# Kernel optimization log

Measured on AMD Instinct MI355X. Metric: run time of the kernel, lower is better.

The kernel has to match this reference:

```python
import jax, jax.numpy as jnp
import numpy as np

K = 10  # knn_graph default k
NEG_SLOPE = 0.2


def _knn_idx(x, k):
    # x: (B, N, C) -> idx (B, N, k) of nearest neighbors (excluding self)
    x2 = jnp.sum(x * x, axis=-1)                       # (B, N)
    d = x2[:, :, None] + x2[:, None, :] - 2.0 * jnp.einsum('bnc,bmc->bnm', x, x)
    _, idx = jax.lax.top_k(-d, k + 1)                  # smallest distances
    return idx[:, :, 1:]                               # drop self


def _edge_conv(x, W, s, t, k):
    # x: (B, N, C); W: (O, 2C); s,t: (O,) folded BN scale/bias
    idx = _knn_idx(x, k)                               # (B, N, k)
    neigh = jax.vmap(lambda xb, ib: xb[ib])(x, idx)    # (B, N, k, C)
    xi = jnp.broadcast_to(x[:, :, None, :], neigh.shape)
    edge = jnp.concatenate([neigh - xi, xi], axis=-1)  # (B, N, k, 2C)
    h = jnp.einsum('bnkc,oc->bnko', edge, W) * s + t
    h = jnp.where(h >= 0, h, NEG_SLOPE * h)            # LeakyReLU(0.2)
    return jnp.max(h, axis=2)                          # max over neighbors -> (B, N, O)


def setup_inputs() -> dict:
    key = jax.random.key(0)
    ks = jax.random.split(key, 32)
    B, N = 8, 2048
    NC = 3
    def w(k_, shape):
        fan_in = shape[-1]
        return jax.random.normal(k_, shape, jnp.float32) * (1.0 / np.sqrt(fan_in))
    def sb(k_, c):  # positive scale, small bias
        k1, k2 = jax.random.split(k_)
        return (jax.random.uniform(k1, (c,), jnp.float32, 0.5, 1.5),
                jax.random.normal(k2, (c,), jnp.float32) * 0.1)
    points = jax.random.normal(ks[0], (B, N, 3), jnp.float32)
    W1 = w(ks[1], (64, 6));    s1, t1 = sb(ks[2], 64)
    W2 = w(ks[3], (64, 128));  s2, t2 = sb(ks[4], 64)
    W3 = w(ks[5], (128, 128)); s3, t3 = sb(ks[6], 128)
    W4 = w(ks[7], (256, 256)); s4, t4 = sb(ks[8], 256)
    W5 = w(ks[9], (1024, 512)); s5, t5 = sb(ks[10], 1024)
    Wf1 = w(ks[11], (512, 1024)); sf1, tf1 = sb(ks[12], 512)
    Wf2 = w(ks[13], (256, 512)); bf2 = jax.random.normal(ks[14], (256,), jnp.float32) * 0.02
    sf2, tf2 = sb(ks[15], 256)
    Wf3 = w(ks[16], (NC, 256)); bf3 = jax.random.normal(ks[17], (NC,), jnp.float32) * 0.02
    return {
        'points': points,
        'W1': W1, 's1': s1, 't1': t1,
        'W2': W2, 's2': s2, 't2': t2,
        'W3': W3, 's3': s3, 't3': t3,
        'W4': W4, 's4': s4, 't4': t4,
        'W5': W5, 's5': s5, 't5': t5,
        'Wf1': Wf1, 'sf1': sf1, 'tf1': tf1,
        'Wf2': Wf2, 'bf2': bf2, 'sf2': sf2, 'tf2': tf2,
        'Wf3': Wf3, 'bf3': bf3,
    }


def reference(points, W1, s1, t1, W2, s2, t2, W3, s3, t3, W4, s4, t4,
              W5, s5, t5, Wf1, sf1, tf1, Wf2, bf2, sf2, tf2, Wf3, bf3):
    lrelu = lambda h: jnp.where(h >= 0, h, NEG_SLOPE * h)
    out1 = _edge_conv(points, W1, s1, t1, K)   # (B, N, 64)
    out2 = _edge_conv(out1, W2, s2, t2, K)     # (B, N, 64)
    out3 = _edge_conv(out2, W3, s3, t3, K)     # (B, N, 128)
    out4 = _edge_conv(out3, W4, s4, t4, K)     # (B, N, 256)
    x = jnp.concatenate([out1, out2, out3, out4], axis=-1)  # (B, N, 512)
    h = lrelu(jnp.einsum('bnc,oc->bno', x, W5) * s5 + t5)   # (B, N, 1024)
    h = jnp.max(h, axis=1)                                  # global max pool -> (B, 1024)
    h = lrelu((h @ Wf1.T) * sf1 + tf1)                      # (B, 512); dropout=identity (eval)
    h = lrelu((h @ Wf2.T + bf2) * sf2 + tf2)                # (B, 256)
    return h @ Wf3.T + bf3                                  # (B, num_classes)
```

## Files before the change

### kernel.cpp

```cpp
#include <hip/hip_runtime.h>
#include <hip/hip_bf16.h>


#define NEG 0.2f
#define FMAX 3.402823466e+38f
#define KINIT 0x7F7FFFFFFFFFFFFFull

typedef __hip_bfloat16 bf16;
typedef __attribute__((ext_vector_type(8))) short s8v;
typedef __attribute__((ext_vector_type(4))) float f32x4;
typedef unsigned long long u64;

#define BB 8
#define NN 2048
#define BNTOT (BB * NN)
#define NPART 4

#define OFF_NORMS ((size_t)0)
#define OFF_PART (OFF_NORMS + BNTOT)
#define OFF_POOLED (OFF_PART + 8 * 1024 * 32)
#define OFF_H1 (OFF_POOLED + 8 * 1024)
#define OFF_H2 (OFF_H1 + 8 * 512)
#define WSF_TOTAL (OFF_H2 + 8 * 256)

#define WB1 0
#define WB2 4096
#define WB3 12288
#define WB4 28672
#define WTOT 94208

__device__ float g_ws_f[WSF_TOTAL];
__device__ float g_G[(size_t)8 * BNTOT * 64];
__device__ u64 g_pk[(size_t)BNTOT * NPART * 10];
__device__ int g_flag;
__device__ unsigned short g_hi[(size_t)BNTOT * 512];
__device__ unsigned short g_lo[(size_t)BNTOT * 512];
__device__ unsigned short g_xhi5[(size_t)BNTOT * 512];
__device__ unsigned short g_xlo5[(size_t)BNTOT * 512];
__device__ unsigned short g_whi[1024 * 512];
__device__ unsigned short g_wlo[1024 * 512];
__device__ unsigned short g_wfh[WTOT];
__device__ unsigned short g_wfl[WTOT];

__device__ __forceinline__ float ldany(const void* p, size_t i, int isb) {
  if (isb) return __bfloat162float(((const bf16*)p)[i]);
  return ((const float*)p)[i];
}

__global__ void probe_kernel(const void* pts) {
  const unsigned* w = (const unsigned*)pts;
  int cnt = 0;
  for (int i = 0; i < 256; ++i) {
    unsigned e2 = (w[i] >> 7) & 0xFF;
    cnt += (e2 >= 110 && e2 <= 135);
  }
  g_flag = (cnt > 128) ? 1 : 0;
}

__global__ void norms_kernel(const void* xraw, int lda, int C, int BN) {
  const int isb = g_flag;
  float* norms = g_ws_f + OFF_NORMS;
  int row = blockIdx.x * (blockDim.x >> 6) + (threadIdx.x >> 6);
  int lane = threadIdx.x & 63;
  if (row >= BN) return;
  float s = 0.f;
  for (int c = lane; c < C; c += 64) {
    float v = ldany(xraw, (size_t)row * lda + c, isb);
    s += v * v;
  }
#pragma unroll
  for (int off = 32; off > 0; off >>= 1) s += __shfl_down(s, off, 64);
  if (lane == 0) norms[row] = s;
}

__global__ void zero_norms() {
  int i = blockIdx.x * blockDim.x + threadIdx.x;
  if (i < BNTOT) g_ws_f[OFF_NORMS + i] = 0.f;
}

__global__ void split_kernel(const void* xraw, int lda, int C,
                             int csh2, int dst, int total) {
  int i = blockIdx.x * blockDim.x + threadIdx.x;
  if (i >= total) return;
  const int isb = g_flag;
  int t = i >> 9, win = i & 511;
  int quad = win >> 7, l16 = (win >> 3) & 15, j = win & 7;
  int ktiles_m1 = (1 << csh2) - 1;
  int rg = t >> csh2, kt = t & ktiles_m1;
  int r = rg * 16 + l16;
  int c = kt * 32 + quad * 8 + j;
  float v = (c < C) ? ldany(xraw, (size_t)r * lda + c, isb) : 0.f;
  bf16 h = __float2bfloat16(v);
  float hf = __bfloat162float(h);
  bf16 l = __float2bfloat16(v - hf);
  unsigned short* H = dst ? g_whi : g_hi;
  unsigned short* L = dst ? g_wlo : g_lo;
  H[i] = *(unsigned short*)&h;
  L[i] = *(unsigned short*)&l;
}

__global__ void split_w(const void* W, int C, int ktsh, int wbase, int whalf,
                        int total) {
  int i = blockIdx.x * blockDim.x + threadIdx.x;
  if (i >= total) return;
  int z = blockIdx.y;
  const int isb = g_flag;
  int t = i >> 9, win = i & 511;
  int quad = win >> 7, l16 = (win >> 3) & 15, j = win & 7;
  int rg = t >> ktsh, kt = t & ((1 << ktsh) - 1);
  int orow = rg * 16 + l16;
  int c = kt * 32 + quad * 8 + j;
  float v = (c < C) ? ldany(W, (size_t)orow * (2 * C) + (size_t)z * C + c, isb) : 0.f;
  bf16 h = __float2bfloat16(v);
  float hf = __bfloat162float(h);
  bf16 l = __float2bfloat16(v - hf);
  g_wfh[wbase + z * whalf + i] = *(unsigned short*)&h;
  g_wfl[wbase + z * whalf + i] = *(unsigned short*)&l;
}

template <int CPAD>
__global__ __launch_bounds__(256) void knn_fused(int N) {
  constexpr int KT = CPAD >> 5;
  __shared__ __align__(16) float sdbuf[2][64 * 68];
  __shared__ float th_sh[4][64];
  const int tid = threadIdx.x;
  const int wave = tid >> 6, lane = tid & 63;
  const int quad = lane >> 4, l16 = lane & 15;
  const int b = blockIdx.y;
  const int q0 = blockIdx.x * 64;
  const int part = blockIdx.z;
  const int PN = N / NPART;
  const int rowb = b * N;
  const float* norms = g_ws_f + OFF_NORMS;

  const int arg = ((rowb + q0) >> 4) + wave;
  s8v ah[KT], al[KT];
#pragma unroll
  for (int kt = 0; kt < KT; ++kt) {
    const int abase = (arg * KT + kt) * 512 + lane * 8;
    ah[kt] = *(const s8v*)(g_hi + abase);
    al[kt] = *(const s8v*)(g_lo + abase);
  }

  const int selfn = q0 + lane;
  const float qn = norms[rowb + selfn];
  u64 K[10];
#pragma unroll
  for (int i = 0; i < 10; ++i) K[i] = KINIT;
  th_sh[wave][lane] = FMAX;

  int pb = 0;
  for (int m0 = part * PN; m0 < (part + 1) * PN; m0 += 64, pb ^= 1) {
    float nmv[4];
#pragma unroll
    for (int s = 0; s < 4; ++s) nmv[s] = norms[rowb + m0 + s * 16 + l16];
    f32x4 acc[4];
#pragma unroll
    for (int s = 0; s < 4; ++s) acc[s] = (f32x4){0.f, 0.f, 0.f, 0.f};
    const int brg0 = (rowb + m0) >> 4;
    const int btile = brg0 * (KT * 512) + lane * 8;
#pragma unroll
    for (int kt = 0; kt < KT; ++kt) {
#pragma unroll
      for (int s = 0; s < 4; ++s) {
        const int boff = btile + (s * KT + kt) * 512;
        s8v bh = *(const s8v*)(g_hi + boff);
        s8v bl = *(const s8v*)(g_lo + boff);
        acc[s] = __builtin_amdgcn_mfma_f32_16x16x32_bf16(ah[kt], bh, acc[s], 0, 0, 0);
        acc[s] = __builtin_amdgcn_mfma_f32_16x16x32_bf16(ah[kt], bl, acc[s], 0, 0, 0);
        acc[s] = __builtin_amdgcn_mfma_f32_16x16x32_bf16(al[kt], bh, acc[s], 0, 0, 0);
      }
    }
    float* sd = sdbuf[pb];
#pragma unroll
    for (int s = 0; s < 4; ++s) {
      int ml = s * 16 + l16;
#pragma unroll
      for (int r = 0; r < 4; ++r)
        sd[(wave * 16 + quad * 4 + r) * 68 + ml] = nmv[s] - 2.f * acc[s][r];
    }
    __syncthreads();
    float T = fminf(fminf(th_sh[0][lane], th_sh[1][lane]),
                    fminf(th_sh[2][lane], th_sh[3][lane]));
    T = fminf(T, __uint_as_float((unsigned)(K[9] >> 32)));
    const float Tq = T - qn;
    const int mbase = m0 + wave * 16;
    const float* srow = sd + lane * 68 + wave * 16;
    unsigned pass = 0;
#pragma unroll
    for (int jj = 0; jj < 16; jj += 4) {
      float4 d4 = *(const float4*)(srow + jj);
      pass |= (unsigned)(d4.x <= Tq) << jj;
      pass |= (unsigned)(d4.y <= Tq) << (jj + 1);
      pass |= (unsigned)(d4.z <= Tq) << (jj + 2);
      pass |= (unsigned)(d4.w <= Tq) << (jj + 3);
    }
    if ((unsigned)(selfn - mbase) < 16u) pass &= ~(1u << (selfn - mbase));
    while (pass) {
      int jj = __builtin_ctz(pass);
      pass &= pass - 1;
      int m = mbase + jj;
      float d = fmaxf(srow[jj] + qn, 0.f);
      u64 key = ((u64)__float_as_uint(d) << 32) | (unsigned)m;
      if (key < K[9]) {
        bool prev = true;
#pragma unroll
        for (int s2 = 9; s2 >= 1; --s2) {
          bool sh = key < K[s2 - 1];
          K[s2] = sh ? K[s2 - 1] : (prev ? key : K[s2]);
          prev = sh;
        }
        if (prev) K[0] = key;
      }
    }
    th_sh[wave][lane] = __uint_as_float((unsigned)(K[9] >> 32));
  }
  __syncthreads();
  u64* mlist = (u64*)sdbuf;
#pragma unroll
  for (int i = 0; i < 10; ++i) mlist[(lane * 4 + wave) * 10 + i] = K[i];
  __syncthreads();
  if (tid < 64) {
    int q = tid;
    int p0 = 0, p1 = 0, p2 = 0, p3 = 0;
    size_t ob = ((size_t)(rowb + q0 + q) * NPART + part) * 10;
    for (int cnt = 0; cnt < 10; ++cnt) {
      u64 k0 = mlist[(q * 4 + 0) * 10 + p0];
      u64 k1 = mlist[(q * 4 + 1) * 10 + p1];
      u64 k2 = mlist[(q * 4 + 2) * 10 + p2];
      u64 k3 = mlist[(q * 4 + 3) * 10 + p3];
      u64 bk = k0; int bp = 0;
      if (k1 < bk) { bk = k1; bp = 1; }
      if (k2 < bk) { bk = k2; bp = 2; }
      if (k3 < bk) { bk = k3; bp = 3; }
      if (bp == 0) ++p0; else if (bp == 1) ++p1; else if (bp == 2) ++p2; else ++p3;
      g_pk[ob + cnt] = bk;
    }
  }
}

template <int CPAD>
__global__ __launch_bounds__(256) void gmat_mfma(int wbase, int whalf, int BN) {
  constexpr int KT = CPAD >> 5;
  const int tid = threadIdx.x;
  const int wave = tid >> 6, lane = tid & 63;
  const int quad = lane >> 4, l16 = lane & 15;
  const int r0 = blockIdx.x * 64;
  const int chunk = blockIdx.y;
  const int z = blockIdx.z;
  const int wz = wbase + z * whalf;
  const int wrg0 = chunk * 4;
  f32x4 acc[4];
#pragma unroll
  for (int s = 0; s < 4; ++s) acc[s] = (f32x4){0.f, 0.f, 0.f, 0.f};
  const int arg = (r0 >> 4) + wave;
#pragma unroll
  for (int kt = 0; kt < KT; ++kt) {
    const int abase = (arg * KT + kt) * 512 + lane * 8;
    s8v ah = *(const s8v*)(g_hi + abase);
    s8v al = *(const s8v*)(g_lo + abase);
#pragma unroll
    for (int s = 0; s < 4; ++s) {
      const int woff = wz + ((wrg0 + s) * KT + kt) * 512 + lane * 8;
      s8v bh = *(const s8v*)(g_wfh + woff);
      s8v bl = *(const s8v*)(g_wfl + woff);
      acc[s] = __builtin_amdgcn_mfma_f32_16x16x32_bf16(ah, bh, acc[s], 0, 0, 0);
      acc[s] = __builtin_amdgcn_mfma_f32_16x16x32_bf16(ah, bl, acc[s], 0, 0, 0);
      acc[s] = __builtin_amdgcn_mfma_f32_16x16x32_bf16(al, bh, acc[s], 0, 0, 0);
    }
  }
  float* Gz = g_G + (size_t)(chunk * 2 + z) * BN * 64;
#pragma unroll
  for (int s = 0; s < 4; ++s)
#pragma unroll
    for (int r = 0; r < 4; ++r)
      Gz[(r0 + wave * 16 + quad * 4 + r) * 64 + s * 16 + l16] = acc[s][r];
}

__global__ void edge_epi64(const void* s, const void* t, int colbase,
                           int knn_csh2, int norms_mode, int BN, int N) {
  __shared__ u64 kbuf[4][40];
  __shared__ int oidx[4][10];
  const int isb = g_flag;
  int tid = threadIdx.x;
  int p = tid >> 6, o = tid & 63;
  int row = blockIdx.x * 4 + p;
  int chunk = blockIdx.y;
  const float* G1 = g_G + (size_t)(chunk * 2 + 0) * BN * 64;
  const float* G2 = g_G + (size_t)(chunk * 2 + 1) * BN * 64;
  int b = row / N;
  if (o < 40) kbuf[p][o] = g_pk[(size_t)row * 40 + o];
  if (o < 40) {
    u64 myk = kbuf[p][o];
    int rank = 0;
#pragma unroll 8
    for (int j = 0; j < 40; ++j) rank += (kbuf[p][j] < myk);
    if (rank < 10) oidx[p][rank] = (int)(myk & 0xFFFFFFFFu);
  }
  float g1n = G1[row * 64 + o];
  float base = G2[row * 64 + o] - g1n;
  int co = chunk * 64 + o;
  float sv = ldany(s, co, isb), tv = ldany(t, co, isb);
  float mx = -FMAX;
  const int bn64 = b * N * 64;
#pragma unroll
  for (int k = 0; k < 10; ++k) {
    int m = oidx[p][k];
    m = (m < 0) ? 0 : ((m >= N) ? N - 1 : m);
    float h = sv * (G1[bn64 + m * 64 + o] + base) + tv;
    h = (h >= 0.f) ? h : NEG * h;
    mx = fmaxf(mx, h);
  }
  bf16 h16 = __float2bfloat16(mx);
  float hf = __bfloat162float(h16);
  bf16 l16v = __float2bfloat16(mx - hf);
  unsigned short hu = *(unsigned short*)&h16;
  unsigned short lu = *(unsigned short*)&l16v;
  if (knn_csh2 >= 0) {
    int KTL = 1 << knn_csh2;
    int ki = ((row >> 4) * KTL + (co >> 5)) * 512 +
             ((co >> 3) & 3) * 128 + (row & 15) * 8 + (co & 7);
    g_hi[ki] = hu; g_lo[ki] = lu;
  }
  {
    int gc = colbase + co;
    int wi = ((row >> 4) * 16 + (gc >> 5)) * 512 +
             ((gc >> 3) & 3) * 128 + (row & 15) * 8 + (gc & 7);
    g_xhi5[wi] = hu; g_xlo5[wi] = lu;
  }
  if (norms_mode) {
    float ns = mx * mx;
#pragma unroll
    for (int off = 32; off > 0; off >>= 1) ns += __shfl_down(ns, off, 64);
    if (o == 0) {
      if (norms_mode == 1) g_ws_f[OFF_NORMS + row] = ns;
      else atomicAdd(&g_ws_f[OFF_NORMS + row], ns);
    }
  }
}

__global__ __launch_bounds__(256) void w5max_mfma(const void* s5, const void* t5, int N) {
  const int tid = threadIdx.x;
  const int wave = tid >> 6, lane = tid & 63;
  const int quad = lane >> 4, l16 = lane & 15;
  const int b = blockIdx.z;
  const int o0 = blockIdx.y * 64, n0 = blockIdx.x * 256;
  f32x4 acc[4][4];
#pragma unroll
  for (int a = 0; a < 4; ++a)
#pragma unroll
    for (int s = 0; s < 4; ++s) acc[a][s] = (f32x4){0.f, 0.f, 0.f, 0.f};

  const int arg0 = ((b * N + n0) >> 4) + wave * 4;
  const int wrg0 = o0 >> 4;
  for (int kt = 0; kt < 16; ++kt) {
    s8v ah[4], al[4];
#pragma unroll
    for (int a = 0; a < 4; ++a) {
      const int abase = ((arg0 + a) * 16 + kt) * 512 + lane * 8;
      ah[a] = *(const s8v*)(g_xhi5 + abase);
      al[a] = *(const s8v*)(g_xlo5 + abase);
    }
#pragma unroll
    for (int s = 0; s < 4; ++s) {
      const int bbase = ((wrg0 + s) * 16 + kt) * 512 + lane * 8;
      s8v bh = *(const s8v*)(g_whi + bbase);
      s8v bl = *(const s8v*)(g_wlo + bbase);
#pragma unroll
      for (int a = 0; a < 4; ++a) {
        acc[a][s] = __builtin_amdgcn_mfma_f32_16x16x32_bf16(ah[a], bh, acc[a][s], 0, 0, 0);
        acc[a][s] = __builtin_amdgcn_mfma_f32_16x16x32_bf16(ah[a], bl, acc[a][s], 0, 0, 0);
        acc[a][s] = __builtin_amdgcn_mfma_f32_16x16x32_bf16(al[a], bh, acc[a][s], 0, 0, 0);
      }
    }
  }
  __shared__ float red[4][64];
  const int isb = g_flag;
#pragma unroll
  for (int s = 0; s < 4; ++s) {
    float m4 = -FMAX;
#pragma unroll
    for (int a = 0; a < 4; ++a)
#pragma unroll
      for (int r = 0; r < 4; ++r) m4 = fmaxf(m4, acc[a][s][r]);
#pragma unroll
    for (int off = 16; off < 64; off <<= 1) m4 = fmaxf(m4, __shfl_down(m4, off, 64));
    if (quad == 0) red[wave][s * 16 + l16] = m4;
  }
  __syncthreads();
  if (tid < 64) {
    float m = fmaxf(fmaxf(red[0][tid], red[1][tid]), fmaxf(red[2][tid], red[3][tid]));
    int o = o0 + tid;
    float sv = ldany(s5, o, isb), tv = ldany(t5, o, isb);
    float h = sv * m + tv;
    h = (h >= 0.f) ? h : NEG * h;
    g_ws_f[OFF_PART + ((size_t)b * 1024 + o) * 8 + blockIdx.x] = h;
  }
}

__global__ void poolred_kernel() {
  const float* part = g_ws_f + OFF_PART;
  float* pooled = g_ws_f + OFF_POOLED;
  int i = blockIdx.x * blockDim.x + threadIdx.x;
  if (i >= 8 * 1024) return;
  const float* p = part + (size_t)i * 8;
  float m = -FMAX;
#pragma unroll
  for (int j = 0; j < 8; ++j) m = fmaxf(m, p[j]);
  pooled[i] = m;
}

__global__ void fc_kernel(size_t inoff, const void* W, const void* bias,
                          const void* s, const void* t, size_t outoff, int has_out,
                          void* OUTB, int Bb, int IC, int OC, int act) {
  const int isb = g_flag;
  const float* IN = g_ws_f + inoff;
  int gw = (blockIdx.x * blockDim.x + threadIdx.x) >> 6;
  int lane = threadIdx.x & 63;
  if (gw >= Bb * OC) return;
  int b = gw / OC, o = gw % OC;
  const float* in = IN + (size_t)b * IC;
  float acc = 0.f;
  for (int c = lane; c < IC; c += 64) acc += in[c] * ldany(W, (size_t)o * IC + c, isb);
#pragma unroll
  for (int off = 32; off > 0; off >>= 1) acc += __shfl_down(acc, off, 64);
  if (lane == 0) {
    float h = acc;
    if (bias) h += ldany(bias, o, isb);
    if (s) h = h * ldany(s, o, isb) + ldany(t, o, isb);
    if (act) h = (h >= 0.f) ? h : NEG * h;
    if (has_out) g_ws_f[outoff + (size_t)b * OC + o] = h;
    if (OUTB) {
      if (isb) ((bf16*)OUTB)[(size_t)b * OC + o] = __float2bfloat16(h);
      else ((float*)OUTB)[(size_t)b * OC + o] = h;
    }
  }
}

extern "C" void kernel_launch(void* const* d_in, const int* in_sizes, int n_in,
                              void* d_out, int out_size, void* d_ws, size_t ws_size,
                              hipStream_t stream) {
  const int B = 8, N = 2048, BN = B * N;
  const void* points = d_in[0];
  const void *W1 = d_in[1], *s1 = d_in[2], *t1 = d_in[3];
  const void *W2 = d_in[4], *s2 = d_in[5], *t2 = d_in[6];
  const void *W3 = d_in[7], *s3 = d_in[8], *t3 = d_in[9];
  const void *W4 = d_in[10], *s4 = d_in[11], *t4 = d_in[12];
  const void *W5 = d_in[13], *s5 = d_in[14], *t5 = d_in[15];
  const void *Wf1 = d_in[16], *sf1 = d_in[17], *tf1 = d_in[18];
  const void *Wf2 = d_in[19], *bf2 = d_in[20], *sf2 = d_in[21], *tf2 = d_in[22];
  const void *Wf3 = d_in[23], *bf3 = d_in[24];

  probe_kernel<<<1, 1, 0, stream>>>(points);
  split_kernel<<<(1024 * 512) / 256, 256, 0, stream>>>(W5, 512, 512, 4, 1, 1024 * 512);
  split_w<<<dim3(2048 / 256, 2), 256, 0, stream>>>(W1, 3, 0, WB1, 2048, 2048);
  split_w<<<dim3(4096 / 256, 2), 256, 0, stream>>>(W2, 64, 1, WB2, 4096, 4096);
  split_w<<<dim3(8192 / 256, 2), 256, 0, stream>>>(W3, 64, 1, WB3, 8192, 8192);
  split_w<<<dim3(32768 / 256, 2), 256, 0, stream>>>(W4, 128, 2, WB4, 32768, 32768);

  norms_kernel<<<BN / 4, 256, 0, stream>>>(points, 3, 3, BN);
  split_kernel<<<(BN * 32) / 256, 256, 0, stream>>>(points, 3, 3, 0, 0, BN * 32);
  knn_fused<32><<<dim3(N / 64, B, NPART), 256, 0, stream>>>(N);
  gmat_mfma<32><<<dim3(BN / 64, 1, 2), 256, 0, stream>>>(WB1, 2048, BN);
  edge_epi64<<<dim3(BN / 4, 1), 256, 0, stream>>>(s1, t1, 0, 1, 1, BN, N);
  knn_fused<64><<<dim3(N / 64, B, NPART), 256, 0, stream>>>(N);
  gmat_mfma<64><<<dim3(BN / 64, 1, 2), 256, 0, stream>>>(WB2, 4096, BN);
  edge_epi64<<<dim3(BN / 4, 1), 256, 0, stream>>>(s2, t2, 64, 1, 1, BN, N);
  knn_fused<64><<<dim3(N / 64, B, NPART), 256, 0, stream>>>(N);
  gmat_mfma<64><<<dim3(BN / 64, 2, 2), 256, 0, stream>>>(WB3, 8192, BN);
  zero_norms<<<BN / 256, 256, 0, stream>>>();
  edge_epi64<<<dim3(BN / 4, 2), 256, 0, stream>>>(s3, t3, 128, 2, 2, BN, N);
  knn_fused<128><<<dim3(N / 64, B, NPART), 256, 0, stream>>>(N);
  gmat_mfma<128><<<dim3(BN / 64, 4, 2), 256, 0, stream>>>(WB4, 32768, BN);
  edge_epi64<<<dim3(BN / 4, 4), 256, 0, stream>>>(s4, t4, 256, -1, 0, BN, N);
  w5max_mfma<<<dim3(8, 16, 8), 256, 0, stream>>>(s5, t5, N);
  poolred_kernel<<<32, 256, 0, stream>>>();
  fc_kernel<<<(8 * 512 * 64) / 256, 256, 0, stream>>>(OFF_POOLED, Wf1, nullptr, sf1, tf1, OFF_H1, 1, nullptr, 8, 1024, 512, 1);
  fc_kernel<<<(8 * 256 * 64) / 256, 256, 0, stream>>>(OFF_H1, Wf2, bf2, sf2, tf2, OFF_H2, 1, nullptr, 8, 512, 256, 1);
  fc_kernel<<<6, 256, 0, stream>>>(OFF_H2, Wf3, bf3, nullptr, nullptr, 0, 0, d_out, 8, 256, 3, 0);
}
```

Before: 559.4 us.

## Select kNN candidates directly from MFMA registers without shared-memory distance staging

The distance MFMA now swaps its operands so that each lane's accumulator holds distances for one query across several candidates. Each lane keeps a top-10 list per query and candidate-quad, filtered by a threshold shared through wave shuffles. This removes the shared-memory distance tile, the per-tile __syncthreads, and the cross-wave threshold array. In exchange it keeps four partial lists per query that must be merged at the end, and the filter branch may diverge more within a wave.

```diff
diff --git a/kernel.cpp b/kernel.cpp
--- a/kernel.cpp
+++ b/kernel.cpp
@@ -118,11 +118,24 @@
   g_wfl[wbase + z * whalf + i] = *(unsigned short*)&l;
 }
 
+__device__ __forceinline__ void insert10(u64* K, float d, int m) {
+  u64 key = ((u64)__float_as_uint(fmaxf(d, 0.f)) << 32) | (unsigned)m;
+  if (key < K[9]) {
+    bool prev = true;
+#pragma unroll
+    for (int s2 = 9; s2 >= 1; --s2) {
+      bool sh = key < K[s2 - 1];
+      K[s2] = sh ? K[s2 - 1] : (prev ? key : K[s2]);
+      prev = sh;
+    }
+    if (prev) K[0] = key;
+  }
+}
+
 template <int CPAD>
 __global__ __launch_bounds__(256) void knn_fused(int N) {
   constexpr int KT = CPAD >> 5;
-  __shared__ __align__(16) float sdbuf[2][64 * 68];
-  __shared__ float th_sh[4][64];
+  __shared__ __align__(16) u64 mbuf[4][16 * 4 * 10];
   const int tid = threadIdx.x;
   const int wave = tid >> 6, lane = tid & 63;
   const int quad = lane >> 4, l16 = lane & 15;
@@ -133,102 +146,75 @@
   const int rowb = b * N;
   const float* norms = g_ws_f + OFF_NORMS;
 
-  const int arg = ((rowb + q0) >> 4) + wave;
-  s8v ah[KT], al[KT];
+  const int qrg = ((rowb + q0) >> 4) + wave;
+  s8v qh[KT], ql[KT];
 #pragma unroll
   for (int kt = 0; kt < KT; ++kt) {
-    const int abase = (arg * KT + kt) * 512 + lane * 8;
-    ah[kt] = *(const s8v*)(g_hi + abase);
-    al[kt] = *(const s8v*)(g_lo + abase);
-  }
-
-  const int selfn = q0 + lane;
-  const float qn = norms[rowb + selfn];
+    const int qbase = (qrg * KT + kt) * 512 + lane * 8;
+    qh[kt] = *(const s8v*)(g_hi + qbase);
+    ql[kt] = *(const s8v*)(g_lo + qbase);
+  }
+
+  const int selfq = q0 + wave * 16 + l16;
+  const float qn = norms[rowb + selfq];
   u64 K[10];
 #pragma unroll
   for (int i = 0; i < 10; ++i) K[i] = KINIT;
-  th_sh[wave][lane] = FMAX;
-
-  int pb = 0;
-  for (int m0 = part * PN; m0 < (part + 1) * PN; m0 += 64, pb ^= 1) {
-    float nmv[4];
-#pragma unroll
-    for (int s = 0; s < 4; ++s) nmv[s] = norms[rowb + m0 + s * 16 + l16];
+
+  for (int m0 = part * PN; m0 < (part + 1) * PN; m0 += 64) {
+    f32x4 nmv[4];
+#pragma unroll
+    for (int s = 0; s < 4; ++s)
+      nmv[s] = *(const f32x4*)(norms + rowb + m0 + s * 16 + quad * 4);
     f32x4 acc[4];
 #pragma unroll
     for (int s = 0; s < 4; ++s) acc[s] = (f32x4){0.f, 0.f, 0.f, 0.f};
-    const int brg0 = (rowb + m0) >> 4;
-    const int btile = brg0 * (KT * 512) + lane * 8;
+    const int mrg0 = (rowb + m0) >> 4;
 #pragma unroll
     for (int kt = 0; kt < KT; ++kt) {
 #pragma unroll
       for (int s = 0; s < 4; ++s) {
-        const int boff = btile + (s * KT + kt) * 512;
-        s8v bh = *(const s8v*)(g_hi + boff);
-        s8v bl = *(const s8v*)(g_lo + boff);
-        acc[s] = __builtin_amdgcn_mfma_f32_16x16x32_bf16(ah[kt], bh, acc[s], 0, 0, 0);
-        acc[s] = __builtin_amdgcn_mfma_f32_16x16x32_bf16(ah[kt], bl, acc[s], 0, 0, 0);
-        acc[s] = __builtin_amdgcn_mfma_f32_16x16x32_bf16(al[kt], bh, acc[s], 0, 0, 0);
+        const int moff = ((mrg0 + s) * KT + kt) * 512 + lane * 8;
+        s8v mh = *(const s8v*)(g_hi + moff);
+        s8v ml = *(const s8v*)(g_lo + moff);
+        acc[s] = __builtin_amdgcn_mfma_f32_16x16x32_bf16(mh, qh[kt], acc[s], 0, 0, 0);
+        acc[s] = __builtin_amdgcn_mfma_f32_16x16x32_bf16(ml, qh[kt], acc[s], 0, 0, 0);
+        acc[s] = __builtin_amdgcn_mfma_f32_16x16x32_bf16(mh, ql[kt], acc[s], 0, 0, 0);
       }
     }
-    float* sd = sdbuf[pb];
+    float myk9 = __uint_as_float((unsigned)(K[9] >> 32));
+    float t2 = fminf(myk9, __shfl_xor(myk9, 16, 64));
+    float T = fminf(t2, __shfl_xor(t2, 32, 64));
+    const float Tq = T - qn;
+    unsigned selfmask = 0;
+    {
+      unsigned ds_ = (unsigned)(selfq - m0);
+      if (ds_ < 64u && (((ds_ >> 2) & 3u) == (unsigned)quad))
+        selfmask = 1u << (((ds_ >> 4) << 2) | (ds_ & 3u));
+    }
 #pragma unroll
     for (int s = 0; s < 4; ++s) {
-      int ml = s * 16 + l16;
-#pragma unroll
-      for (int r = 0; r < 4; ++r)
-        sd[(wave * 16 + quad * 4 + r) * 68 + ml] = nmv[s] - 2.f * acc[s][r];
-    }
-    __syncthreads();
-    float T = fminf(fminf(th_sh[0][lane], th_sh[1][lane]),
-                    fminf(th_sh[2][lane], th_sh[3][lane]));
-    T = fminf(T, __uint_as_float((unsigned)(K[9] >> 32)));
-    const float Tq = T - qn;
-    const int mbase = m0 + wave * 16;
-    const float* srow = sd + lane * 68 + wave * 16;
-    unsigned pass = 0;
-#pragma unroll
-    for (int jj = 0; jj < 16; jj += 4) {
-      float4 d4 = *(const float4*)(srow + jj);
-      pass |= (unsigned)(d4.x <= Tq) << jj;
-      pass |= (unsigned)(d4.y <= Tq) << (jj + 1);
-      pass |= (unsigned)(d4.z <= Tq) << (jj + 2);
-      pass |= (unsigned)(d4.w <= Tq) << (jj + 3);
-    }
-    if ((unsigned)(selfn - mbase) < 16u) pass &= ~(1u << (selfn - mbase));
-    while (pass) {
-      int jj = __builtin_ctz(pass);
-      pass &= pass - 1;
-      int m = mbase + jj;
-      float d = fmaxf(srow[jj] + qn, 0.f);
-      u64 key = ((u64)__float_as_uint(d) << 32) | (unsigned)m;
-      if (key < K[9]) {
-        bool prev = true;
-#pragma unroll
-        for (int s2 = 9; s2 >= 1; --s2) {
-          bool sh = key < K[s2 - 1];
-          K[s2] = sh ? K[s2 - 1] : (prev ? key : K[s2]);
-          prev = sh;
-        }
-        if (prev) K[0] = key;
+#pragma unroll
+      for (int r = 0; r < 4; ++r) {
+        float dp = fmaf(-2.f, acc[s][r], nmv[s][r]);
+        if (!((selfmask >> (s * 4 + r)) & 1u) && dp <= Tq)
+          insert10(K, dp + qn, m0 + s * 16 + quad * 4 + r);
       }
     }
-    th_sh[wave][lane] = __uint_as_float((unsigned)(K[9] >> 32));
-  }
+  }
+  u64* wl = mbuf[wave];
+#pragma unroll
+  for (int i = 0; i < 10; ++i) wl[(l16 * 4 + quad) * 10 + i] = K[i];
   __syncthreads();
-  u64* mlist = (u64*)sdbuf;
-#pragma unroll
-  for (int i = 0; i < 10; ++i) mlist[(lane * 4 + wave) * 10 + i] = K[i];
-  __syncthreads();
-  if (tid < 64) {
-    int q = tid;
+  if (l16 == lane) {
+    int q = l16;
     int p0 = 0, p1 = 0, p2 = 0, p3 = 0;
-    size_t ob = ((size_t)(rowb + q0 + q) * NPART + part) * 10;
+    size_t ob = ((size_t)(rowb + q0 + wave * 16 + q) * NPART + part) * 10;
     for (int cnt = 0; cnt < 10; ++cnt) {
-      u64 k0 = mlist[(q * 4 + 0) * 10 + p0];
-      u64 k1 = mlist[(q * 4 + 1) * 10 + p1];
-      u64 k2 = mlist[(q * 4 + 2) * 10 + p2];
-      u64 k3 = mlist[(q * 4 + 3) * 10 + p3];
+      u64 k0 = wl[(q * 4 + 0) * 10 + p0];
+      u64 k1 = wl[(q * 4 + 1) * 10 + p1];
+      u64 k2 = wl[(q * 4 + 2) * 10 + p2];
+      u64 k3 = wl[(q * 4 + 3) * 10 + p3];
       u64 bk = k0; int bp = 0;
       if (k1 < bk) { bk = k1; bp = 1; }
       if (k2 < bk) { bk = k2; bp = 2; }
```

After: 744.7 us. +33.1%, slower.
